# Optimization experiments

Hardware: AMD Instinct MI355X
Metric: run time of the kernel (lower is better)

Reference implementation:

```python
import jax, jax.numpy as jnp
import numpy as np

N = 50000      # num_nodes
E = 800000     # num_edges
F = 29         # num_node_features
IN = F + 3     # in_channels after hstack with pos
H = 64         # hidden_dim
B = 50         # batch_size (num graphs)
L = 7          # num GINConv layers


def setup_inputs() -> dict:
    key = jax.random.key(0)
    ks = jax.random.split(key, 12)
    s_in = 1.0 / np.sqrt(IN)
    s_h = 1.0 / np.sqrt(H)
    return {
        "x": jax.random.normal(ks[0], (N, F), jnp.float32),
        "pos": jax.random.normal(ks[1], (N, 3), jnp.float32),
        "edge_index": jax.random.randint(ks[2], (2, E), 0, N),
        "batch": jnp.sort(jax.random.randint(ks[3], (N,), 0, B)),
        # GINConv l: MLP = Linear(in,H) -> ReLU -> Linear(H,H)
        "W1_first": jax.random.normal(ks[4], (IN, H), jnp.float32) * s_in,
        "W1_rest": jax.random.normal(ks[5], (L - 1, H, H), jnp.float32) * s_h,
        "b1": jax.random.normal(ks[6], (L, H), jnp.float32) * 0.01,
        "W2": jax.random.normal(ks[7], (L, H, H), jnp.float32) * s_h,
        "b2": jax.random.normal(ks[8], (L, H), jnp.float32) * 0.01,
        "lin_w": jax.random.normal(ks[9], (H, 1), jnp.float32) * s_h,
        "lin_b": jax.random.normal(ks[10], (1,), jnp.float32) * 0.01,
    }


def reference(x, pos, edge_index, batch, W1_first, W1_rest, b1, W2, b2, lin_w, lin_b):
    src, dst = edge_index[0], edge_index[1]
    h = jnp.concatenate([x, pos], axis=1)  # [N, IN]

    def gin_conv(h, Wa, ba, Wb, bb):
        # sum aggregation of source features at destination nodes, eps=0
        agg = jax.ops.segment_sum(h[src], dst, num_segments=N)
        z = h + agg
        z = jax.nn.relu(z @ Wa + ba)
        return z @ Wb + bb

    h = jax.nn.relu(gin_conv(h, W1_first, b1[0], W2[0], b2[0]))
    for l in range(1, L):
        h = gin_conv(h, W1_rest[l - 1], b1[l], W2[l], b2[l])
        if l < L - 1:  # no activation after last conv (jk=None)
            h = jax.nn.relu(h)

    # global mean pool per graph
    sums = jax.ops.segment_sum(h, batch, num_segments=B)            # [B, H]
    counts = jax.ops.segment_sum(jnp.ones((N,), h.dtype), batch, num_segments=B)
    pooled = sums / jnp.maximum(counts, 1.0)[:, None]

    return pooled @ lin_w + lin_b  # [B, 1]
```

## Files before the change

kernel.cpp:

```cpp
#include <hip/hip_runtime.h>
#include <stdint.h>

#define NF 29
#define HD 64
#define NL 7
#define LDW 72
#define NCHUNK 256
#define BSH 8
#define PER_M (64 * LDW)

typedef __attribute__((ext_vector_type(8))) __bf16 bf16x8;
typedef __attribute__((ext_vector_type(4))) float floatx4;
typedef int int32x4 __attribute__((ext_vector_type(4)));
typedef float f32x4v __attribute__((ext_vector_type(4)));

extern "C" __device__ f32x4v llvm_amdgcn_raw_buffer_load_fp32x4(
    int32x4 srsrc, int voffset, int soffset, int cachepolicy)
    __asm("llvm.amdgcn.raw.buffer.load.v4f32");

__device__ __forceinline__ int32x4 make_srd(const void* p) {
    unsigned long long a = (unsigned long long)p;
    int32x4 r;
    r.x = (int)(a & 0xFFFFFFFFull);
    r.y = (int)(a >> 32);
    r.z = -1;
    r.w = 0x00020000;
    return r;
}
__device__ __forceinline__ uint4 bload16_sc0(int32x4 srd, int voff) {
    f32x4v v = llvm_amdgcn_raw_buffer_load_fp32x4(srd, voff, 0, 1 );
    union { f32x4v f; uint4 u; } c;
    c.f = v;
    return c.u;
}

__device__ __forceinline__ unsigned short f2bf(float x) {
    unsigned u = __float_as_uint(x);
    unsigned r = (u + 0x7fffu + ((u >> 16) & 1u)) >> 16;
    return (unsigned short)r;
}
__device__ __forceinline__ unsigned pack_bf2(float x, float y) {
    return (unsigned)f2bf(x) | ((unsigned)f2bf(y) << 16);
}
__device__ __forceinline__ float bflo(uint32_t u) { return __uint_as_float(u << 16); }
__device__ __forceinline__ float bfhi(uint32_t u) { return __uint_as_float(u & 0xffff0000u); }
__device__ __forceinline__ float bf2f(unsigned short s) {
    return __uint_as_float((uint32_t)s << 16);
}

__global__ void init_kernel(const float* __restrict__ x, const float* __restrict__ pos,
                            unsigned short* __restrict__ h0,
                            const float* __restrict__ W1f, const float* __restrict__ W1r,
                            const float* __restrict__ W2, unsigned short* __restrict__ wpk,
                            int N) {
    int t = blockIdx.x * blockDim.x + threadIdx.x;
    if (t < NL * 2 * PER_M) {
        int l = t / (2 * PER_M);
        int r = t - l * 2 * PER_M;
        int m = r / PER_M;
        int q = r - m * PER_M;
        int j = q / LDW, k = q - j * LDW;
        float v = 0.f;
        if (m == 0) {
            int ind = (l == 0) ? 32 : 64;
            if (k < ind) v = (l == 0) ? W1f[k * 64 + j]
                                      : W1r[(size_t)(l - 1) * 4096 + (size_t)k * 64 + j];
        } else {
            if (k < 64) v = W2[(size_t)l * 4096 + (size_t)k * 64 + j];
        }
        wpk[t] = f2bf(v);
    }
    if (t < N * 32) {
        int n = t >> 5, f = t & 31;
        float v = (f < NF) ? x[n * NF + f] : pos[n * 3 + (f - NF)];
        h0[t] = f2bf(v);
    }
}

__global__ void bucket_hist_kernel(const int* __restrict__ dst, int E, int chunk,
                                   int* __restrict__ bcnt, int* __restrict__ bsum) {
    __shared__ int hist[256];
    int tid = threadIdx.x;
    hist[tid] = 0;
    __syncthreads();
    int lo = blockIdx.x * chunk, hi = min(E, lo + chunk);
    for (int e = lo + tid; e < hi; e += 256) atomicAdd(&hist[dst[e] >> BSH], 1);
    __syncthreads();
    bcnt[tid * NCHUNK + blockIdx.x] = hist[tid];
    if (hist[tid]) atomicAdd(&bsum[tid], hist[tid]);
}

__global__ void bstart_scan_kernel(const int* __restrict__ bsum, int* __restrict__ bstart,
                                   int* __restrict__ rowptr, int nbuk, int N, int E) {
    __shared__ int s[256];
    int t = threadIdx.x;
    s[t] = (t < nbuk) ? bsum[t] : 0;
    __syncthreads();
    for (int off = 1; off < 256; off <<= 1) {
        int v = (t >= off) ? s[t - off] : 0;
        __syncthreads();
        s[t] += v;
        __syncthreads();
    }
    bstart[t] = (t == 0) ? 0 : s[t - 1];
    if (t == 255) bstart[256] = s[255];
    if (t == 0) rowptr[N] = E;
}

__global__ void bucket_off_kernel(const int* __restrict__ bcnt, const int* __restrict__ bstart,
                                  int* __restrict__ boffT) {
    __shared__ int s[256];
    int b = blockIdx.x, t = threadIdx.x;
    int c = bcnt[b * NCHUNK + t];
    s[t] = c;
    __syncthreads();
    for (int off = 1; off < 256; off <<= 1) {
        int v = (t >= off) ? s[t - off] : 0;
        __syncthreads();
        s[t] += v;
        __syncthreads();
    }
    int excl = s[t] - c;
    boffT[t * 256 + b] = bstart[b] + excl;
}

__global__ void bucket_scatter_kernel(const int* __restrict__ src, const int* __restrict__ dst,
                                      int E, int chunk, const int* __restrict__ boffT,
                                      unsigned int* __restrict__ ebuf) {
    __shared__ int cur[256];
    int tid = threadIdx.x, c = blockIdx.x;
    cur[tid] = boffT[c * 256 + tid];
    __syncthreads();
    int lo = c * chunk, hi = min(E, lo + chunk);
    for (int e = lo + tid; e < hi; e += 256) {
        int d = dst[e];
        int p = atomicAdd(&cur[d >> BSH], 1);
        ebuf[p] = (unsigned int)src[e] | ((unsigned int)(d & 255) << 16);
    }
}

__global__ void final_scatter_kernel(const unsigned int* __restrict__ ebuf,
                                     const int* __restrict__ bstart,
                                     int* __restrict__ rowptr,
                                     unsigned short* __restrict__ colsrc, int N) {
    __shared__ int cnt[256];
    __shared__ int cur[256];
    __shared__ int s[256];
    int b = blockIdx.x, t = threadIdx.x;
    cnt[t] = 0;
    __syncthreads();
    int lo = bstart[b], hi = bstart[b + 1];
    for (int e = lo + t; e < hi; e += 256) atomicAdd(&cnt[ebuf[e] >> 16], 1);
    __syncthreads();
    int c = cnt[t];
    s[t] = c;
    __syncthreads();
    for (int off = 1; off < 256; off <<= 1) {
        int v = (t >= off) ? s[t - off] : 0;
        __syncthreads();
        s[t] += v;
        __syncthreads();
    }
    int base = lo + s[t] - c;
    int node = (b << BSH) + t;
    if (node < N) rowptr[node] = base;
    cur[t] = base;
    __syncthreads();
    for (int e = lo + t; e < hi; e += 256) {
        unsigned int ed = ebuf[e];
        int p = atomicAdd(&cur[ed >> 16], 1);
        colsrc[p] = (unsigned short)(ed & 0xffffu);
    }
}

template<int IND, bool RELU_OUT, bool LAST>
__global__ __launch_bounds__(512, 8)
void gin_layer_kernel(const unsigned short* __restrict__ hin,
                      const int* __restrict__ rowptr, const unsigned short* __restrict__ colsrc,
                      const unsigned short* __restrict__ wAT, const unsigned short* __restrict__ wBT,
                      const float* __restrict__ ba, const float* __restrict__ bb,
                      unsigned short* __restrict__ hout,
                      const int* __restrict__ batch, float* __restrict__ pool,
                      int N)
{
    __shared__ __align__(16) unsigned short zbuf[64 * LDW];
    __shared__ __align__(16) unsigned short t1buf[64 * LDW];

    const int tid = threadIdx.x;
    const int lane = tid & 63;
    const int w = tid >> 6;
    const int tile0 = blockIdx.x * 64;

    const int32x4 srd = make_srd(hin);
    const int g = lane >> 3;
    const int j = lane & 7;
    const int node = tile0 + w * 8 + g;

    int rp;
    {
        int idx = tile0 + w * 8 + (lane < 9 ? lane : 8);
        if (idx > N) idx = N;
        rp = rowptr[idx];
    }
    int e0 = __shfl(rp, g);
    int e1 = __shfl(rp, g + 1);
    if (node >= N) { e0 = 0; e1 = 0; }

    float acc[8] = {0.f, 0.f, 0.f, 0.f, 0.f, 0.f, 0.f, 0.f};
    auto addrow = [&](uint4 u) {
        acc[0] += bflo(u.x); acc[1] += bfhi(u.x);
        acc[2] += bflo(u.y); acc[3] += bfhi(u.y);
        acc[4] += bflo(u.z); acc[5] += bfhi(u.z);
        acc[6] += bflo(u.w); acc[7] += bfhi(u.w);
    };

    if constexpr (IND == 64) {
        const int f4 = lane & 7;
        if (node < N) addrow(bload16_sc0(srd, node * 128 + f4 * 16));
        int e = e0;
        int idxv = (e + j < e1) ? (int)colsrc[e + j] : 0;
        for (; e + 7 < e1; e += 8) {
            int en = e + 8;
            int idx_next = (en + j < e1) ? (int)colsrc[en + j] : 0;
            int s[8];
            #pragma unroll
            for (int q = 0; q < 8; ++q) s[q] = __shfl(idxv, g * 8 + q);
            uint4 u[8];
            #pragma unroll
            for (int q = 0; q < 8; ++q) u[q] = bload16_sc0(srd, s[q] * 128 + f4 * 16);
            #pragma unroll
            for (int q = 0; q < 8; ++q) addrow(u[q]);
            idxv = idx_next;
        }
        {
            int rem = e1 - e;
            #pragma unroll
            for (int q = 0; q < 8; ++q) {
                if (q < rem) {
                    int s = __shfl(idxv, g * 8 + q);
                    addrow(bload16_sc0(srd, s * 128 + f4 * 16));
                }
            }
        }
        uint4 pk;
        pk.x = pack_bf2(acc[0], acc[1]); pk.y = pack_bf2(acc[2], acc[3]);
        pk.z = pack_bf2(acc[4], acc[5]); pk.w = pack_bf2(acc[6], acc[7]);
        *(uint4*)&zbuf[(w * 8 + g) * LDW + f4 * 8] = pk;
    } else {
        const int p = (lane >> 2) & 1;
        const int f4 = lane & 3;
        if (node < N && p == 0) addrow(bload16_sc0(srd, node * 64 + f4 * 16));
        int e = e0 + p;
        for (; e + 7 < e1; e += 8) {
            int s0 = colsrc[e], s1 = colsrc[e + 2], s2 = colsrc[e + 4], s3 = colsrc[e + 6];
            uint4 u0 = bload16_sc0(srd, s0 * 64 + f4 * 16);
            uint4 u1 = bload16_sc0(srd, s1 * 64 + f4 * 16);
            uint4 u2 = bload16_sc0(srd, s2 * 64 + f4 * 16);
            uint4 u3 = bload16_sc0(srd, s3 * 64 + f4 * 16);
            addrow(u0); addrow(u1); addrow(u2); addrow(u3);
        }
        while (e < e1) { addrow(bload16_sc0(srd, (int)colsrc[e] * 64 + f4 * 16)); e += 2; }
        #pragma unroll
        for (int i = 0; i < 8; ++i) acc[i] += __shfl_xor(acc[i], 4);
        if (p == 0) {
            uint4 pk;
            pk.x = pack_bf2(acc[0], acc[1]); pk.y = pack_bf2(acc[2], acc[3]);
            pk.z = pack_bf2(acc[4], acc[5]); pk.w = pack_bf2(acc[6], acc[7]);
            *(uint4*)&zbuf[(w * 8 + g) * LDW + f4 * 8] = pk;
        }
    }
    __syncthreads();

    const int n0 = lane & 15, quad = lane >> 4;
    const int stripe = w & 3, jhalf = w >> 2;
    const int row0 = stripe * 16;
    const int jt0 = jhalf * 2, jt1 = jhalf * 2 + 1;

    floatx4 c0, c1;
    {
        float b0v = ba[jt0 * 16 + n0], b1v = ba[jt1 * 16 + n0];
        c0 = (floatx4){b0v, b0v, b0v, b0v};
        c1 = (floatx4){b1v, b1v, b1v, b1v};
    }
    #pragma unroll
    for (int kk = 0; kk < IND / 32; ++kk) {
        bf16x8 a   = *(const bf16x8*)&zbuf[(row0 + n0) * LDW + kk * 32 + quad * 8];
        bf16x8 br0 = *(const bf16x8*)&wAT[(jt0 * 16 + n0) * LDW + kk * 32 + quad * 8];
        bf16x8 br1 = *(const bf16x8*)&wAT[(jt1 * 16 + n0) * LDW + kk * 32 + quad * 8];
        c0 = __builtin_amdgcn_mfma_f32_16x16x32_bf16(a, br0, c0, 0, 0, 0);
        c1 = __builtin_amdgcn_mfma_f32_16x16x32_bf16(a, br1, c1, 0, 0, 0);
    }
    #pragma unroll
    for (int r = 0; r < 4; ++r) {
        int row = row0 + quad * 4 + r;
        t1buf[row * LDW + jt0 * 16 + n0] = f2bf(fmaxf(c0[r], 0.f));
        t1buf[row * LDW + jt1 * 16 + n0] = f2bf(fmaxf(c1[r], 0.f));
    }
    __syncthreads();

    {
        float b0v = bb[jt0 * 16 + n0], b1v = bb[jt1 * 16 + n0];
        c0 = (floatx4){b0v, b0v, b0v, b0v};
        c1 = (floatx4){b1v, b1v, b1v, b1v};
    }
    #pragma unroll
    for (int kk = 0; kk < 2; ++kk) {
        bf16x8 a   = *(const bf16x8*)&t1buf[(row0 + n0) * LDW + kk * 32 + quad * 8];
        bf16x8 br0 = *(const bf16x8*)&wBT[(jt0 * 16 + n0) * LDW + kk * 32 + quad * 8];
        bf16x8 br1 = *(const bf16x8*)&wBT[(jt1 * 16 + n0) * LDW + kk * 32 + quad * 8];
        c0 = __builtin_amdgcn_mfma_f32_16x16x32_bf16(a, br0, c0, 0, 0, 0);
        c1 = __builtin_amdgcn_mfma_f32_16x16x32_bf16(a, br1, c1, 0, 0, 0);
    }
    #pragma unroll
    for (int r = 0; r < 4; ++r) {
        int row = row0 + quad * 4 + r;
        float v0 = c0[r], v1 = c1[r];
        if (RELU_OUT) { v0 = fmaxf(v0, 0.f); v1 = fmaxf(v1, 0.f); }
        zbuf[row * LDW + jt0 * 16 + n0] = f2bf(v0);
        zbuf[row * LDW + jt1 * 16 + n0] = f2bf(v1);
    }
    __syncthreads();

    if constexpr (!LAST) {
        int nl = tid >> 3, c4 = tid & 7;
        int nodeo = tile0 + nl;
        if (nodeo < N) {
            uint4 v = *(const uint4*)&zbuf[nl * LDW + c4 * 8];
            ((uint4*)hout)[(size_t)nodeo * 8 + c4] = v;
        }
    } else {
        int nl0 = w * 8;
        int bvec = 0;
        if (lane < 8) {
            int idx = tile0 + nl0 + lane;
            bvec = batch[idx < N ? idx : (N - 1)];
        }
        int bsel = -1;
        float run = 0.f;
        for (int i = 0; i < 8; ++i) {
            int nodeo = tile0 + nl0 + i;
            if (nodeo >= N) break;
            int b = __shfl(bvec, i);
            float v = bf2f(zbuf[(nl0 + i) * LDW + lane]);
            if (b != bsel) {
                if (bsel >= 0) atomicAdd(&pool[bsel * HD + lane], run);
                bsel = b; run = 0.f;
            }
            run += v;
        }
        if (bsel >= 0) atomicAdd(&pool[bsel * HD + lane], run);
    }
}

__global__ void final_kernel(const float* __restrict__ pool, const int* __restrict__ batch,
                             const float* __restrict__ lin_w, const float* __restrict__ lin_b,
                             float* __restrict__ out, int B, int N) {
    int b = blockIdx.x;
    int lane = threadIdx.x;
    int lo = 0, hi = N;
    while (lo < hi) { int m = (lo + hi) >> 1; if (batch[m] < b) lo = m + 1; else hi = m; }
    int lb = lo;
    lo = 0; hi = N;
    while (lo < hi) { int m = (lo + hi) >> 1; if (batch[m] <= b) lo = m + 1; else hi = m; }
    float c = fmaxf((float)(lo - lb), 1.f);
    float v = pool[b * HD + lane] / c * lin_w[lane];
    for (int off = 32; off > 0; off >>= 1) v += __shfl_down(v, off);
    if (lane == 0) out[b] = v + lin_b[0];
}

extern "C" void kernel_launch(void* const* d_in, const int* in_sizes, int n_in,
                              void* d_out, int out_size, void* d_ws, size_t ws_size,
                              hipStream_t stream)
{
    const float* x   = (const float*)d_in[0];
    const float* pos = (const float*)d_in[1];
    const int*  eidx = (const int*)d_in[2];
    const int* batch = (const int*)d_in[3];
    const float* W1f = (const float*)d_in[4];
    const float* W1r = (const float*)d_in[5];
    const float* b1  = (const float*)d_in[6];
    const float* W2  = (const float*)d_in[7];
    const float* b2  = (const float*)d_in[8];
    const float* lw  = (const float*)d_in[9];
    const float* lb  = (const float*)d_in[10];

    int N = in_sizes[3];
    int E = in_sizes[2] / 2;
    int B = out_size;
    const int* src = eidx;
    const int* dst = eidx + E;

    char* ws = (char*)d_ws;
    size_t off = 0;
    auto alloc = [&](size_t bytes) -> void* {
        void* p = ws + off;
        off += (bytes + 255) & ~(size_t)255;
        return p;
    };
    unsigned short* bufA = (unsigned short*)alloc((size_t)N * HD * 2);
    unsigned short* bufB = (unsigned short*)alloc((size_t)N * HD * 2);
    int*   rowptr = (int*)  alloc((size_t)(N + 1) * 4);
    unsigned short* colsrc = (unsigned short*)alloc((size_t)E * 2);
    unsigned int* ebuf = (unsigned int*)alloc((size_t)E * 4);
    float* pool   = (float*)alloc((size_t)B * HD * 4);
    int*   bcnt   = (int*)  alloc((size_t)256 * NCHUNK * 4);
    int*   boffT  = (int*)  alloc((size_t)NCHUNK * 256 * 4);
    int*   bsum   = (int*)  alloc(256 * 4);
    int*   bstart = (int*)  alloc(257 * 4);
    unsigned short* wpk = (unsigned short*)alloc((size_t)NL * 2 * PER_M * 2);

    hipMemsetAsync(bsum, 0, 256 * 4, stream);
    hipMemsetAsync(pool, 0, (size_t)B * HD * 4, stream);

    int nbuk = (N + 255) >> BSH;
    int chunk = (E + NCHUNK - 1) / NCHUNK;

    init_kernel<<<(N * 32 + 255) / 256, 256, 0, stream>>>(x, pos, bufA, W1f, W1r, W2, wpk, N);
    bucket_hist_kernel<<<NCHUNK, 256, 0, stream>>>(dst, E, chunk, bcnt, bsum);
    bstart_scan_kernel<<<1, 256, 0, stream>>>(bsum, bstart, rowptr, nbuk, N, E);
    bucket_off_kernel<<<nbuk, 256, 0, stream>>>(bcnt, bstart, boffT);
    bucket_scatter_kernel<<<NCHUNK, 256, 0, stream>>>(src, dst, E, chunk, boffT, ebuf);
    final_scatter_kernel<<<nbuk, 256, 0, stream>>>(ebuf, bstart, rowptr, colsrc, N);

    const int gblocks = (N + 63) / 64;
    gin_layer_kernel<32, true, false><<<gblocks, 512, 0, stream>>>(
        bufA, rowptr, colsrc, wpk + 0 * PER_M, wpk + 1 * PER_M, b1, b2, bufB,
        nullptr, nullptr, N);
    unsigned short* cur_in = bufB;
    unsigned short* cur_out = bufA;
    for (int l = 1; l < NL; ++l) {
        const unsigned short* wa = wpk + (size_t)(2 * l + 0) * PER_M;
        const unsigned short* wb = wpk + (size_t)(2 * l + 1) * PER_M;
        const float* ba = b1 + l * HD;
        const float* bb = b2 + l * HD;
        if (l < NL - 1) {
            gin_layer_kernel<HD, true, false><<<gblocks, 512, 0, stream>>>(
                cur_in, rowptr, colsrc, wa, wb, ba, bb, cur_out, nullptr, nullptr, N);
            unsigned short* tmp = cur_in; cur_in = cur_out; cur_out = tmp;
        } else {
            gin_layer_kernel<HD, false, true><<<gblocks, 512, 0, stream>>>(
                cur_in, rowptr, colsrc, wa, wb, ba, bb, nullptr, batch, pool, N);
        }
    }
    final_kernel<<<B, 64, 0, stream>>>(pool, batch, lw, lb, (float*)d_out, B, N);
}
```

Baseline: 256.8 us.

## Merge init, histogram and pool-clear into one front kernel; drop scan kernel

Folds the input conversion, weight packing, pool zeroing and edge bucket histogram into a single launch, partitioned by block index. The single-block bucket-start scan kernel is removed: bucket_off and final_scatter now each compute their own bucket start with a block-local reduction over bsum. The h0 conversion now writes 8 packed bf16 values per thread as a uint4 instead of one value per thread. This cuts launch count and a serialized tiny kernel, at the cost of redundant per-block reductions.

```diff
diff --git a/kernel.cpp b/kernel.cpp
--- a/kernel.cpp
+++ b/kernel.cpp
@@ -48,53 +48,86 @@
     return __uint_as_float((uint32_t)s << 16);
 }
 
-__global__ void init_kernel(const float* __restrict__ x, const float* __restrict__ pos,
-                            unsigned short* __restrict__ h0,
-                            const float* __restrict__ W1f, const float* __restrict__ W1r,
-                            const float* __restrict__ W2, unsigned short* __restrict__ wpk,
-                            int N) {
-    int t = blockIdx.x * blockDim.x + threadIdx.x;
-    if (t < NL * 2 * PER_M) {
-        int l = t / (2 * PER_M);
-        int r = t - l * 2 * PER_M;
-        int m = r / PER_M;
-        int q = r - m * PER_M;
-        int j = q / LDW, k = q - j * LDW;
-        float v = 0.f;
-        if (m == 0) {
-            int ind = (l == 0) ? 32 : 64;
-            if (k < ind) v = (l == 0) ? W1f[k * 64 + j]
-                                      : W1r[(size_t)(l - 1) * 4096 + (size_t)k * 64 + j];
-        } else {
-            if (k < 64) v = W2[(size_t)l * 4096 + (size_t)k * 64 + j];
-        }
-        wpk[t] = f2bf(v);
-    }
-    if (t < N * 32) {
-        int n = t >> 5, f = t & 31;
-        float v = (f < NF) ? x[n * NF + f] : pos[n * 3 + (f - NF)];
-        h0[t] = f2bf(v);
-    }
-}
-
-__global__ void bucket_hist_kernel(const int* __restrict__ dst, int E, int chunk,
-                                   int* __restrict__ bcnt, int* __restrict__ bsum) {
+__global__ void front_kernel(const float* __restrict__ x, const float* __restrict__ pos,
+                             unsigned short* __restrict__ h0,
+                             const float* __restrict__ W1f, const float* __restrict__ W1r,
+                             const float* __restrict__ W2, unsigned short* __restrict__ wpk,
+                             const int* __restrict__ dst, int E, int chunk,
+                             int* __restrict__ bcnt, int* __restrict__ bsum,
+                             float* __restrict__ pool, int N, int B) {
     __shared__ int hist[256];
-    int tid = threadIdx.x;
-    hist[tid] = 0;
-    __syncthreads();
-    int lo = blockIdx.x * chunk, hi = min(E, lo + chunk);
-    for (int e = lo + tid; e < hi; e += 256) atomicAdd(&hist[dst[e] >> BSH], 1);
-    __syncthreads();
-    bcnt[tid * NCHUNK + blockIdx.x] = hist[tid];
-    if (hist[tid]) atomicAdd(&bsum[tid], hist[tid]);
-}
-
-__global__ void bstart_scan_kernel(const int* __restrict__ bsum, int* __restrict__ bstart,
-                                   int* __restrict__ rowptr, int nbuk, int N, int E) {
+    const int H0B = (N * 4 + 255) / 256;
+    const int WPB = (NL * 2 * PER_M + 255) / 256;
+    int blk = blockIdx.x;
+    if (blk < H0B) {
+        int t = blk * 256 + threadIdx.x;
+        if (t < N * 4) {
+            int n = t >> 2, q = t & 3;
+            const float* xr = x + (size_t)n * NF;
+            float f[8];
+            if (q < 3) {
+                #pragma unroll
+                for (int i = 0; i < 8; ++i) f[i] = xr[q * 8 + i];
+            } else {
+                #pragma unroll
+                for (int i = 0; i < 5; ++i) f[i] = xr[24 + i];
+                f[5] = pos[n * 3 + 0]; f[6] = pos[n * 3 + 1]; f[7] = pos[n * 3 + 2];
+            }
+            uint4 pk;
+            pk.x = pack_bf2(f[0], f[1]); pk.y = pack_bf2(f[2], f[3]);
+            pk.z = pack_bf2(f[4], f[5]); pk.w = pack_bf2(f[6], f[7]);
+            ((uint4*)h0)[t] = pk;
+        }
+    } else if (blk < H0B + WPB) {
+        int bw = blk - H0B;
+        if (bw == 0) {
+            for (int i = threadIdx.x; i < B * HD; i += 256) pool[i] = 0.f;
+        }
+        int t = bw * 256 + threadIdx.x;
+        if (t < NL * 2 * PER_M) {
+            int l = t / (2 * PER_M);
+            int r = t - l * 2 * PER_M;
+            int m = r / PER_M;
+            int q = r - m * PER_M;
+            int j = q / LDW, k = q - j * LDW;
+            float v = 0.f;
+            if (m == 0) {
+                int ind = (l == 0) ? 32 : 64;
+                if (k < ind) v = (l == 0) ? W1f[k * 64 + j]
+                                          : W1r[(size_t)(l - 1) * 4096 + (size_t)k * 64 + j];
+            } else {
+                if (k < 64) v = W2[(size_t)l * 4096 + (size_t)k * 64 + j];
+            }
+            wpk[t] = f2bf(v);
+        }
+    } else {
+        int c = blk - H0B - WPB;
+        int tid = threadIdx.x;
+        hist[tid] = 0;
+        __syncthreads();
+        int lo = c * chunk, hi = min(E, lo + chunk);
+        for (int e = lo + tid; e < hi; e += 256) atomicAdd(&hist[dst[e] >> BSH], 1);
+        __syncthreads();
+        bcnt[tid * NCHUNK + c] = hist[tid];
+        if (hist[tid]) atomicAdd(&bsum[tid], hist[tid]);
+    }
+}
+
+__global__ void bucket_off_kernel(const int* __restrict__ bcnt, const int* __restrict__ bsum,
+                                  int* __restrict__ boffT) {
+    __shared__ int red[256];
     __shared__ int s[256];
-    int t = threadIdx.x;
-    s[t] = (t < nbuk) ? bsum[t] : 0;
+    int b = blockIdx.x, t = threadIdx.x;
+    red[t] = (t < b) ? bsum[t] : 0;
+    __syncthreads();
+    #pragma unroll
+    for (int off = 128; off > 0; off >>= 1) {
+        if (t < off) red[t] += red[t + off];
+        __syncthreads();
+    }
+    int bstart_b = red[0];
+    int c = bcnt[b * NCHUNK + t];
+    s[t] = c;
     __syncthreads();
     for (int off = 1; off < 256; off <<= 1) {
         int v = (t >= off) ? s[t - off] : 0;
@@ -102,26 +135,8 @@
         s[t] += v;
         __syncthreads();
     }
-    bstart[t] = (t == 0) ? 0 : s[t - 1];
-    if (t == 255) bstart[256] = s[255];
-    if (t == 0) rowptr[N] = E;
-}
-
-__global__ void bucket_off_kernel(const int* __restrict__ bcnt, const int* __restrict__ bstart,
-                                  int* __restrict__ boffT) {
-    __shared__ int s[256];
-    int b = blockIdx.x, t = threadIdx.x;
-    int c = bcnt[b * NCHUNK + t];
-    s[t] = c;
-    __syncthreads();
-    for (int off = 1; off < 256; off <<= 1) {
-        int v = (t >= off) ? s[t - off] : 0;
-        __syncthreads();
-        s[t] += v;
-        __syncthreads();
-    }
     int excl = s[t] - c;
-    boffT[t * 256 + b] = bstart[b] + excl;
+    boffT[t * 256 + b] = bstart_b + excl;
 }
 
 __global__ void bucket_scatter_kernel(const int* __restrict__ src, const int* __restrict__ dst,
@@ -140,16 +155,25 @@
 }
 
 __global__ void final_scatter_kernel(const unsigned int* __restrict__ ebuf,
-                                     const int* __restrict__ bstart,
+                                     const int* __restrict__ bsum,
                                      int* __restrict__ rowptr,
-                                     unsigned short* __restrict__ colsrc, int N) {
+                                     unsigned short* __restrict__ colsrc, int N, int E) {
+    __shared__ int red[256];
     __shared__ int cnt[256];
     __shared__ int cur[256];
     __shared__ int s[256];
     int b = blockIdx.x, t = threadIdx.x;
+    red[t] = (t < b) ? bsum[t] : 0;
     cnt[t] = 0;
     __syncthreads();
-    int lo = bstart[b], hi = bstart[b + 1];
+    #pragma unroll
+    for (int off = 128; off > 0; off >>= 1) {
+        if (t < off) red[t] += red[t + off];
+        __syncthreads();
+    }
+    int lo = red[0];
+    int hi = lo + bsum[b];
+    if (b == 0 && t == 0) rowptr[N] = E;
     for (int e = lo + t; e < hi; e += 256) atomicAdd(&cnt[ebuf[e] >> 16], 1);
     __syncthreads();
     int c = cnt[t];
@@ -406,21 +430,20 @@
     int*   bcnt   = (int*)  alloc((size_t)256 * NCHUNK * 4);
     int*   boffT  = (int*)  alloc((size_t)NCHUNK * 256 * 4);
     int*   bsum   = (int*)  alloc(256 * 4);
-    int*   bstart = (int*)  alloc(257 * 4);
     unsigned short* wpk = (unsigned short*)alloc((size_t)NL * 2 * PER_M * 2);
 
     hipMemsetAsync(bsum, 0, 256 * 4, stream);
-    hipMemsetAsync(pool, 0, (size_t)B * HD * 4, stream);
 
     int nbuk = (N + 255) >> BSH;
     int chunk = (E + NCHUNK - 1) / NCHUNK;
 
-    init_kernel<<<(N * 32 + 255) / 256, 256, 0, stream>>>(x, pos, bufA, W1f, W1r, W2, wpk, N);
-    bucket_hist_kernel<<<NCHUNK, 256, 0, stream>>>(dst, E, chunk, bcnt, bsum);
-    bstart_scan_kernel<<<1, 256, 0, stream>>>(bsum, bstart, rowptr, nbuk, N, E);
-    bucket_off_kernel<<<nbuk, 256, 0, stream>>>(bcnt, bstart, boffT);
+    const int H0B = (N * 4 + 255) / 256;
+    const int WPB = (NL * 2 * PER_M + 255) / 256;
+    front_kernel<<<H0B + WPB + NCHUNK, 256, 0, stream>>>(
+        x, pos, bufA, W1f, W1r, W2, wpk, dst, E, chunk, bcnt, bsum, pool, N, B);
+    bucket_off_kernel<<<nbuk, 256, 0, stream>>>(bcnt, bsum, boffT);
     bucket_scatter_kernel<<<NCHUNK, 256, 0, stream>>>(src, dst, E, chunk, boffT, ebuf);
-    final_scatter_kernel<<<nbuk, 256, 0, stream>>>(ebuf, bstart, rowptr, colsrc, N);
+    final_scatter_kernel<<<nbuk, 256, 0, stream>>>(ebuf, bsum, rowptr, colsrc, N, E);
 
     const int gblocks = (N + 63) / 64;
     gin_layer_kernel<32, true, false><<<gblocks, 512, 0, stream>>>(
```

Result: faster. 250.4 us (-2.5%).
